# Optimization experiments

Measured on AMD Instinct MI355X. Metric: run time of the kernel, lower is better.

## Reference

```python
import jax, jax.numpy as jnp
from jax import lax
import numpy as np

C = 64      # channels
K = 3       # dynamic kernel size
N = 2       # batch
H = 256
W = 256
DOWN = 4    # avgpool factor


def _conv(x, w, b):
    # 'SAME' padding matches get_same_padding for odd kernels, dilation=1
    y = lax.conv_general_dilated(x, w, (1, 1), 'SAME',
                                 dimension_numbers=('NCHW', 'OIHW', 'NCHW'))
    return y + b[None, :, None, None]


def _resblock(x, w1, b1, w2, b2):
    out = jax.nn.leaky_relu(_conv(x, w1, b1), 0.1)
    return _conv(out, w2, b2) + x


def _block(x, ws1, bs1, ws2, bs2):
    # fixed small loop over 3 structurally distinct ResBlocks
    for i in range(ws1.shape[0]):
        x = _resblock(x, ws1[i], bs1[i], ws2[i], bs2[i])
    return x


def _avgpool(x, k):
    n, c, h, w = x.shape
    return x.reshape(n, c, h // k, k, w // k, k).mean(axis=(3, 5))


def _maxpool(x, k):
    n, c, h, w = x.shape
    return x.reshape(n, c, h // k, k, w // k, k).max(axis=(3, 5))


def _dyn_conv(x, wt, k):
    # per-pixel depthwise conv: out[n,c,h,w] = sum_{dh,dw} xpad[n,c,h+dh,w+dw] * wt[n, c*k*k + dh*k + dw, h, w]
    # (torch's unfold/permute flattening pairs feat tap (dh,dw) with kernel channel index dh*k+dw)
    n, c, h, w = x.shape
    pad = (k - 1) // 2
    xp = jnp.pad(x, ((0, 0), (0, 0), (pad, pad), (pad, pad)), mode='edge')  # replicate pad
    wr = wt.reshape(n, c, k * k, h, w)
    out = jnp.zeros_like(x)
    for dh in range(k):            # fixed 3x3 tap loop; avoids materializing the unfold tensor
        for dw in range(k):
            out = out + xp[:, :, dh:dh + h, dw:dw + w] * wr[:, :, dh * k + dw]
    return out


def setup_inputs() -> dict:
    key = jax.random.key(0)
    ks = jax.random.split(key, 11)
    s = 0.05  # small init so 6 residual blocks stay numerically tame
    return {
        'x': jax.random.normal(ks[0], (N, C, H, W), jnp.float32),
        'blk1_w1': jax.random.normal(ks[1], (3, C, C, K, K), jnp.float32) * s,
        'blk1_b1': jnp.zeros((3, C), jnp.float32),
        'blk1_w2': jax.random.normal(ks[2], (3, C, C, K, K), jnp.float32) * s,
        'blk1_b2': jnp.zeros((3, C), jnp.float32),
        'blk2_w1': jax.random.normal(ks[3], (3, C, C, K, K), jnp.float32) * s,
        'blk2_b1': jnp.zeros((3, C), jnp.float32),
        'blk2_w2': jax.random.normal(ks[4], (3, C, C, K, K), jnp.float32) * s,
        'blk2_b2': jnp.zeros((3, C), jnp.float32),
        'tok_w': jax.random.normal(ks[5], (K * K * C, C, 1, 1), jnp.float32) * s,
        'tok_b': jnp.zeros((K * K * C,), jnp.float32),
    }


def reference(x, blk1_w1, blk1_b1, blk1_w2, blk1_b2,
              blk2_w1, blk2_b1, blk2_w2, blk2_b2, tok_w, tok_b):
    y = _avgpool(x, DOWN)                                   # [N,C,H/4,W/4]
    y = _block(y, blk1_w1, blk1_b1, blk1_w2, blk1_b2)
    y = _maxpool(y, 2)                                      # [N,C,H/8,W/8]
    y = _block(y, blk2_w1, blk2_b1, blk2_w2, blk2_b2)
    wt = _conv(y, tok_w, tok_b)                             # [N,9C,H/8,W/8]
    n, ck2, hs, ws = wt.shape
    # F.interpolate(scale_factor=2*down, mode='bilinear', align_corners=False)
    wt = jax.image.resize(wt, (n, ck2, hs * 2 * DOWN, ws * 2 * DOWN), method='bilinear')
    return _dyn_conv(x, wt, K)
```

## Files before the change

kernel.cpp:

```cpp
#include <hip/hip_runtime.h>


__global__ __launch_bounds__(256) void avgpool4_k(const float* __restrict__ x,
                                                  float* __restrict__ y) {
    int idx = blockIdx.x * 256 + threadIdx.x;
    int wo = idx & 63;
    int ho = (idx >> 6) & 63;
    int cz = idx >> 12;
    const float* base = x + ((long)cz * 256 + ho * 4) * 256 + wo * 4;
    float s = 0.f;
#pragma unroll
    for (int r = 0; r < 4; ++r) {
        float4 v = *(const float4*)(base + r * 256);
        s += v.x + v.y + v.z + v.w;
    }
    y[idx] = s * 0.0625f;
}

__global__ __launch_bounds__(256) void maxpool2_k(const float* __restrict__ x,
                                                  float* __restrict__ y) {
    int idx = blockIdx.x * 256 + threadIdx.x;
    int wo = idx & 31;
    int ho = (idx >> 5) & 31;
    int cz = idx >> 10;
    const float* base = x + ((long)cz * 64 + ho * 2) * 64 + wo * 2;
    float a = base[0], b = base[1], c = base[64], d = base[65];
    y[idx] = fmaxf(fmaxf(a, b), fmaxf(c, d));
}

template <int S, int OCB>
__global__ __launch_bounds__(256) void conv3x3_t(
    const float* __restrict__ in, const float* __restrict__ wgt,
    const float* __restrict__ bias, const float* __restrict__ res,
    float* __restrict__ out, int lrelu) {
    __shared__ __align__(16) float s_w[64 * 9 * OCB];
    __shared__ float s_in[16 * 342];
    const int tid = threadIdx.x;
    const int tx = tid & 15;
    const int ty = tid >> 4;
    const int tw = blockIdx.x * 16, th = blockIdx.y * 16;
    const int n = blockIdx.z / (64 / OCB);
    const int oc0 = (blockIdx.z % (64 / OCB)) * OCB;

    for (int idx = tid; idx < OCB * 576; idx += 256) {
        int k = idx / 576;
        int r = idx - k * 576;
        int ci = r / 9;
        int tap = r - ci * 9;
        s_w[(ci * 9 + tap) * OCB + k] = wgt[(long)oc0 * 576 + idx];
    }

    constexpr int NLD = 21;
    int g_off[NLD];
    int l_off[NLD];
    unsigned vmask = 0;
#pragma unroll
    for (int j = 0; j < NLD; ++j) {
        int idx = tid + j * 256;
        int t = idx < 5184 ? idx : 5183;
        int ci = t / 324;
        int rem = t - ci * 324;
        int r = rem / 18;
        int c = rem - r * 18;
        int gh = th + r - 1, gw = tw + c - 1;
        if (idx < 5184 && (unsigned)gh < (unsigned)S && (unsigned)gw < (unsigned)S)
            vmask |= (1u << j);
        int ghc = gh < 0 ? 0 : (gh > S - 1 ? S - 1 : gh);
        int gwc = gw < 0 ? 0 : (gw > S - 1 ? S - 1 : gw);
        g_off[j] = ci * S * S + ghc * S + gwc;
        l_off[j] = ci * 342 + r * 19 + c;
    }

    const float* inb = in + (long)n * 64 * S * S;
    float pf[NLD];
#pragma unroll
    for (int j = 0; j < NLD; ++j) pf[j] = inb[g_off[j]];

    float acc[OCB];
#pragma unroll
    for (int k = 0; k < OCB; ++k) acc[k] = 0.f;

    for (int chunk = 0; chunk < 64; chunk += 16) {
        __syncthreads();
#pragma unroll
        for (int j = 0; j < NLD; ++j) {
            float v = ((vmask >> j) & 1u) ? pf[j] : 0.f;
            if (j < 20 || tid < 64) s_in[l_off[j]] = v;
        }
        __syncthreads();
        if (chunk + 16 < 64) {
            const float* nb = inb + (chunk + 16) * S * S;
#pragma unroll
            for (int j = 0; j < NLD; ++j) pf[j] = nb[g_off[j]];
        }
#pragma unroll 4
        for (int ci = 0; ci < 16; ++ci) {
            const float* sp = &s_in[ci * 342 + ty * 19 + tx];
            float xw[9];
#pragma unroll
            for (int r = 0; r < 3; ++r)
#pragma unroll
                for (int c = 0; c < 3; ++c)
                    xw[r * 3 + c] = sp[r * 19 + c];
            const float* wp = &s_w[(chunk + ci) * 9 * OCB];
#pragma unroll
            for (int t = 0; t < 9; ++t) {
                float xv = xw[t];
                if constexpr (OCB == 4) {
                    float4 wv = *(const float4*)&wp[t * 4];
                    acc[0] += xv * wv.x;
                    acc[1] += xv * wv.y;
                    acc[2] += xv * wv.z;
                    acc[3] += xv * wv.w;
                } else {
                    float2 wv = *(const float2*)&wp[t * 2];
                    acc[0] += xv * wv.x;
                    acc[1] += xv * wv.y;
                }
            }
        }
    }

    const int h = th + ty, w = tw + tx;
#pragma unroll
    for (int k = 0; k < OCB; ++k) {
        int oc = oc0 + k;
        float v = acc[k] + bias[oc];
        if (lrelu) v = v > 0.f ? v : 0.1f * v;
        long off = ((long)(n * 64 + oc) * S + h) * S + w;
        if (res) v += res[off];
        out[off] = v;
    }
}

__global__ __launch_bounds__(256) void conv1x1_k(
    const float* __restrict__ in, const float* __restrict__ w,
    const float* __restrict__ b, float* __restrict__ out) {
    __shared__ float s_in[32 * 256];
    __shared__ __align__(16) float s_w[64 * 8];
    const int tid = threadIdx.x;
    const int p0 = blockIdx.x * 256;
    const int cog = blockIdx.y;
    const int n = blockIdx.z;

    for (int idx = tid; idx < 512; idx += 256) {
        int j = idx >> 6;
        int ci = idx & 63;
        s_w[ci * 8 + j] = w[(long)cog * 512 + idx];
    }

    float acc[8];
#pragma unroll
    for (int i = 0; i < 8; ++i) acc[i] = b[cog * 8 + i];

    float pf[32];
#pragma unroll
    for (int i = 0; i < 32; ++i)
        pf[i] = in[(long)(n * 64 + i) * 1024 + p0 + tid];

    for (int chunk = 0; chunk < 64; chunk += 32) {
        __syncthreads();
#pragma unroll
        for (int i = 0; i < 32; ++i) s_in[i * 256 + tid] = pf[i];
        __syncthreads();
        if (chunk + 32 < 64) {
#pragma unroll
            for (int i = 0; i < 32; ++i)
                pf[i] = in[(long)(n * 64 + chunk + 32 + i) * 1024 + p0 + tid];
        }
#pragma unroll 4
        for (int ci = 0; ci < 32; ++ci) {
            float v = s_in[ci * 256 + tid];
            float4 w0 = *(const float4*)&s_w[(chunk + ci) * 8];
            float4 w1 = *(const float4*)&s_w[(chunk + ci) * 8 + 4];
            acc[0] += v * w0.x; acc[1] += v * w0.y;
            acc[2] += v * w0.z; acc[3] += v * w0.w;
            acc[4] += v * w1.x; acc[5] += v * w1.y;
            acc[6] += v * w1.z; acc[7] += v * w1.w;
        }
    }
#pragma unroll
    for (int oc = 0; oc < 8; ++oc)
        out[(long)(n * 576 + cog * 8 + oc) * 1024 + p0 + tid] = acc[oc];
}

__global__ __launch_bounds__(256) void dynconv_k(
    const float* __restrict__ x, const float* __restrict__ wt,
    float* __restrict__ out) {
    __shared__ __align__(16) float s_x[10 * 132];
    const int tid = threadIdx.x;
    const int tx = tid & 31;
    const int ty = tid >> 5;
    const int tw = (blockIdx.x & 1) * 128;
    const int th = (blockIdx.x >> 1) * 8;
    const int cz = blockIdx.y;

    const float* xb = x + (long)cz * 65536;
    for (int idx = tid; idx < 1300; idx += 256) {
        int r = idx / 130;
        int c = idx - r * 130;
        int gh = min(max(th + r - 1, 0), 255);
        int gw = min(max(tw + c - 1, 0), 255);
        s_x[r * 132 + c] = xb[gh * 256 + gw];
    }

    const int h = th + ty;
    const int wbase = tw + tx * 4;

    float src_h = h * 0.125f - 0.4375f;
    int h0 = (int)floorf(src_h);
    float fh = src_h - (float)h0;
    int h0c = min(max(h0, 0), 31), h1c = min(max(h0 + 1, 0), 31);
    float src_w = wbase * 0.125f - 0.4375f;
    int w0 = (int)floorf(src_w);
    float fw0 = src_w - (float)w0;
    int w0c = min(max(w0, 0), 31), w1c = min(max(w0 + 1, 0), 31);

    __syncthreads();

    float vals[3][6];
#pragma unroll
    for (int r = 0; r < 3; ++r) {
        const float* rp = &s_x[(ty + r) * 132 + tx * 4];
        float4 a = *(const float4*)rp;
        float2 b = *(const float2*)(rp + 4);
        vals[r][0] = a.x; vals[r][1] = a.y; vals[r][2] = a.z;
        vals[r][3] = a.w; vals[r][4] = b.x; vals[r][5] = b.y;
    }

    const float* wtb = wt + (long)cz * 9 * 1024;
    float acc[4] = {0.f, 0.f, 0.f, 0.f};
#pragma unroll
    for (int dh = 0; dh < 3; ++dh)
#pragma unroll
        for (int dw = 0; dw < 3; ++dw) {
            const float* p = wtb + (dh * 3 + dw) * 1024;
            float w00 = p[h0c * 32 + w0c], w01 = p[h0c * 32 + w1c];
            float w10 = p[h1c * 32 + w0c], w11 = p[h1c * 32 + w1c];
            float c0 = w00 + fh * (w10 - w00);
            float c1 = w01 + fh * (w11 - w01);
            float d = c1 - c0;
#pragma unroll
            for (int j = 0; j < 4; ++j) {
                float wv = c0 + (fw0 + 0.125f * j) * d;
                acc[j] += vals[dh][j + dw] * wv;
            }
        }

    float4 o;
    o.x = acc[0]; o.y = acc[1]; o.z = acc[2]; o.w = acc[3];
    *(float4*)&out[(long)cz * 65536 + h * 256 + wbase] = o;
}

extern "C" void kernel_launch(void* const* d_in, const int* in_sizes, int n_in,
                              void* d_out, int out_size, void* d_ws, size_t ws_size,
                              hipStream_t stream) {
    const float* x    = (const float*)d_in[0];
    const float* b1w1 = (const float*)d_in[1];
    const float* b1b1 = (const float*)d_in[2];
    const float* b1w2 = (const float*)d_in[3];
    const float* b1b2 = (const float*)d_in[4];
    const float* b2w1 = (const float*)d_in[5];
    const float* b2b1 = (const float*)d_in[6];
    const float* b2w2 = (const float*)d_in[7];
    const float* b2b2 = (const float*)d_in[8];
    const float* tokw = (const float*)d_in[9];
    const float* tokb = (const float*)d_in[10];
    float* out = (float*)d_out;
    float* ws = (float*)d_ws;

    float* A = ws;
    float* B = ws + 524288;
    float* T = ws + 1048576;
    float* P = ws;
    float* Q = ws + 131072;
    float* U = ws + 262144;
    float* WT = ws + 393216;

    const int WSZ = 64 * 64 * 9;

    avgpool4_k<<<2048, 256, 0, stream>>>(x, A);

    dim3 g64(4, 4, 32);
    conv3x3_t<64, 4><<<g64, 256, 0, stream>>>(A, b1w1 + 0 * WSZ, b1b1 + 0,   nullptr, T, 1);
    conv3x3_t<64, 4><<<g64, 256, 0, stream>>>(T, b1w2 + 0 * WSZ, b1b2 + 0,   A,       B, 0);
    conv3x3_t<64, 4><<<g64, 256, 0, stream>>>(B, b1w1 + 1 * WSZ, b1b1 + 64,  nullptr, T, 1);
    conv3x3_t<64, 4><<<g64, 256, 0, stream>>>(T, b1w2 + 1 * WSZ, b1b2 + 64,  B,       A, 0);
    conv3x3_t<64, 4><<<g64, 256, 0, stream>>>(A, b1w1 + 2 * WSZ, b1b1 + 128, nullptr, T, 1);
    conv3x3_t<64, 4><<<g64, 256, 0, stream>>>(T, b1w2 + 2 * WSZ, b1b2 + 128, A,       B, 0);

    maxpool2_k<<<512, 256, 0, stream>>>(B, P);

    dim3 g32(2, 2, 64);
    conv3x3_t<32, 2><<<g32, 256, 0, stream>>>(P, b2w1 + 0 * WSZ, b2b1 + 0,   nullptr, U, 1);
    conv3x3_t<32, 2><<<g32, 256, 0, stream>>>(U, b2w2 + 0 * WSZ, b2b2 + 0,   P,       Q, 0);
    conv3x3_t<32, 2><<<g32, 256, 0, stream>>>(Q, b2w1 + 1 * WSZ, b2b1 + 64,  nullptr, U, 1);
    conv3x3_t<32, 2><<<g32, 256, 0, stream>>>(U, b2w2 + 1 * WSZ, b2b2 + 64,  Q,       P, 0);
    conv3x3_t<32, 2><<<g32, 256, 0, stream>>>(P, b2w1 + 2 * WSZ, b2b1 + 128, nullptr, U, 1);
    conv3x3_t<32, 2><<<g32, 256, 0, stream>>>(U, b2w2 + 2 * WSZ, b2b2 + 128, P,       Q, 0);

    conv1x1_k<<<dim3(4, 72, 2), 256, 0, stream>>>(Q, tokw, tokb, WT);

    dynconv_k<<<dim3(64, 128), 256, 0, stream>>>(x, WT, out);
}
```

Measured before the change: 411.1 us.

## Split 64x64 convs over input-channel slices with fused partial-sum epilogue

Replaces the stage-1 3x3 convolutions with a split-K kernel. Each block handles 16 input channels for 4 output channels on a 32x32 tile and writes a partial sum. The next conv, or the maxpool, sums the four partials, then adds bias, leaky-relu and the residual while loading its input. The residual stream is written as a side output by the ocg==0 blocks. This raises block count and parallelism, and it removes the separate epilogue pass. The cost is extra global traffic, because four partial buffers are read by every consumer block, and the four-way summation is recomputed across output-channel groups.

After: 680.1 us. 1.65x slower.

```diff
diff --git a/kernel.cpp b/kernel.cpp
--- a/kernel.cpp
+++ b/kernel.cpp
@@ -17,15 +17,139 @@
     y[idx] = s * 0.0625f;
 }
 
-__global__ __launch_bounds__(256) void maxpool2_k(const float* __restrict__ x,
-                                                  float* __restrict__ y) {
+__global__ __launch_bounds__(256) void conv64s_k(
+    const float* __restrict__ in0, long pstride,
+    const float* __restrict__ sbias, int slrelu,
+    const float* __restrict__ sres,
+    float* __restrict__ sidew,
+    const float* __restrict__ wgt,
+    float* __restrict__ outp) {
+    __shared__ __align__(16) float s_x[8 * 34 * 36];
+    __shared__ __align__(16) float s_w[16 * 9 * 4];
+    const int tid = threadIdx.x;
+    const int b = blockIdx.x;
+    const int tg = b & 7;
+    const int slot = b >> 3;
+    const int n = tg >> 2;
+    const int tile = tg & 3;
+    const int tx0 = (tile & 1) * 32, ty0 = (tile >> 1) * 32;
+    const int ocg = slot & 15, ks = slot >> 4;
+    const int oc0 = ocg * 4;
+
+    for (int i = tid; i < 576; i += 256) {
+        int k = i / 144;
+        int rem = i - k * 144;
+        int ci = rem / 9;
+        int tap = rem - ci * 9;
+        s_w[(ci * 9 + tap) * 4 + k] =
+            wgt[(oc0 + k) * 576 + (ks * 16 + ci) * 9 + tap];
+    }
+
+    const int ntask = (tid < 16) ? 2 : 1;
+    int t_ci[2], t_j[2];
+    t_ci[0] = tid / 34;  t_j[0] = tid - t_ci[0] * 34;
+    t_ci[1] = (256 + tid) / 34; t_j[1] = (256 + tid) - t_ci[1] * 34;
+
+    const int tx = tid & 7;
+    const int ty = tid >> 3;
+    const int px0 = tx * 4;
+
+    float acc[4][4];
+#pragma unroll
+    for (int k = 0; k < 4; ++k)
+#pragma unroll
+        for (int p = 0; p < 4; ++p) acc[k][p] = 0.f;
+
+    for (int cc = 0; cc < 2; ++cc) {
+        if (cc) __syncthreads();
+        for (int t = 0; t < ntask; ++t) {
+            const int ci = t_ci[t], j = t_j[t];
+            const int ch = ks * 16 + cc * 8 + ci;
+            const int gcol = tx0 + j - 1;
+            const bool colin = (unsigned)gcol < 64u;
+            const long chbase = (long)(n * 64 + ch) * 4096;
+            float bch = 0.f;
+            if (pstride && colin) bch = sbias[ch];
+            float* sp = &s_x[(ci * 34) * 36 + j];
+#pragma unroll 2
+            for (int r = 0; r < 34; ++r) {
+                const int grow = ty0 + r - 1;
+                float v = 0.f;
+                if (colin && (unsigned)grow < 64u) {
+                    const long off = chbase + grow * 64 + gcol;
+                    if (pstride) {
+                        v = in0[off] + in0[off + pstride] +
+                            in0[off + 2 * pstride] + in0[off + 3 * pstride] + bch;
+                        if (slrelu) v = v > 0.f ? v : 0.1f * v;
+                        if (sres) v += sres[off];
+                        if (sidew && ocg == 0) sidew[off] = v;
+                    } else {
+                        v = in0[off];
+                    }
+                }
+                sp[r * 36] = v;
+            }
+        }
+        __syncthreads();
+#pragma unroll 2
+        for (int ci = 0; ci < 8; ++ci) {
+            float xr[3][6];
+#pragma unroll
+            for (int r3 = 0; r3 < 3; ++r3) {
+                const float* rp = &s_x[(ci * 34 + ty + r3) * 36 + px0];
+                float4 a = *(const float4*)rp;
+                float2 e = *(const float2*)(rp + 4);
+                xr[r3][0] = a.x; xr[r3][1] = a.y; xr[r3][2] = a.z;
+                xr[r3][3] = a.w; xr[r3][4] = e.x; xr[r3][5] = e.y;
+            }
+            const int cif = cc * 8 + ci;
+#pragma unroll
+            for (int dh = 0; dh < 3; ++dh)
+#pragma unroll
+                for (int dw = 0; dw < 3; ++dw) {
+                    float4 wv = *(const float4*)&s_w[(cif * 9 + dh * 3 + dw) * 4];
+#pragma unroll
+                    for (int p = 0; p < 4; ++p) {
+                        float xv = xr[dh][p + dw];
+                        acc[0][p] += xv * wv.x;
+                        acc[1][p] += xv * wv.y;
+                        acc[2][p] += xv * wv.z;
+                        acc[3][p] += xv * wv.w;
+                    }
+                }
+        }
+    }
+
+    const int gy = ty0 + ty, gx = tx0 + px0;
+#pragma unroll
+    for (int k = 0; k < 4; ++k) {
+        float4 v;
+        v.x = acc[k][0]; v.y = acc[k][1]; v.z = acc[k][2]; v.w = acc[k][3];
+        long off = (long)ks * 524288 +
+                   ((long)(n * 64 + oc0 + k) * 64 + gy) * 64 + gx;
+        *(float4*)&outp[off] = v;
+    }
+}
+
+__global__ __launch_bounds__(256) void maxpool_comb_k(
+    const float* __restrict__ Pb, const float* __restrict__ bias,
+    const float* __restrict__ res, float* __restrict__ P) {
     int idx = blockIdx.x * 256 + threadIdx.x;
     int wo = idx & 31;
     int ho = (idx >> 5) & 31;
     int cz = idx >> 10;
-    const float* base = x + ((long)cz * 64 + ho * 2) * 64 + wo * 2;
-    float a = base[0], b = base[1], c = base[64], d = base[65];
-    y[idx] = fmaxf(fmaxf(a, b), fmaxf(c, d));
+    float bch = bias[cz & 63];
+    float m = -3.4e38f;
+#pragma unroll
+    for (int dh = 0; dh < 2; ++dh)
+#pragma unroll
+        for (int dw = 0; dw < 2; ++dw) {
+            long off = ((long)cz * 64 + ho * 2 + dh) * 64 + wo * 2 + dw;
+            float y = Pb[off] + Pb[off + 524288] + Pb[off + 1048576] +
+                      Pb[off + 1572864] + bch + res[off];
+            m = fmaxf(m, y);
+        }
+    P[idx] = m;
 }
 
 template <int S, int OCB>
@@ -269,27 +393,29 @@
     float* out = (float*)d_out;
     float* ws = (float*)d_ws;
 
-    float* A = ws;
-    float* B = ws + 524288;
-    float* T = ws + 1048576;
-    float* P = ws;
-    float* Q = ws + 131072;
-    float* U = ws + 262144;
-    float* WT = ws + 393216;
+    float* A  = ws;
+    float* Y1 = ws + 524288;
+    float* Y2 = ws + 1048576;
+    float* Pa = ws + 1572864;
+    float* Pb = ws + 3670016;
+    float* P  = ws + 5767168;
+    float* Q  = ws + 5898240;
+    float* U  = ws + 6029312;
+    float* WT = ws + 6160384;
 
     const int WSZ = 64 * 64 * 9;
+    const long PS = 524288;
 
     avgpool4_k<<<2048, 256, 0, stream>>>(x, A);
 
-    dim3 g64(4, 4, 32);
-    conv3x3_t<64, 4><<<g64, 256, 0, stream>>>(A, b1w1 + 0 * WSZ, b1b1 + 0,   nullptr, T, 1);
-    conv3x3_t<64, 4><<<g64, 256, 0, stream>>>(T, b1w2 + 0 * WSZ, b1b2 + 0,   A,       B, 0);
-    conv3x3_t<64, 4><<<g64, 256, 0, stream>>>(B, b1w1 + 1 * WSZ, b1b1 + 64,  nullptr, T, 1);
-    conv3x3_t<64, 4><<<g64, 256, 0, stream>>>(T, b1w2 + 1 * WSZ, b1b2 + 64,  B,       A, 0);
-    conv3x3_t<64, 4><<<g64, 256, 0, stream>>>(A, b1w1 + 2 * WSZ, b1b1 + 128, nullptr, T, 1);
-    conv3x3_t<64, 4><<<g64, 256, 0, stream>>>(T, b1w2 + 2 * WSZ, b1b2 + 128, A,       B, 0);
-
-    maxpool2_k<<<512, 256, 0, stream>>>(B, P);
+    conv64s_k<<<512, 256, 0, stream>>>(A,  0,  nullptr,      0, nullptr, nullptr, b1w1 + 0 * WSZ, Pa);
+    conv64s_k<<<512, 256, 0, stream>>>(Pa, PS, b1b1 + 0,     1, nullptr, nullptr, b1w2 + 0 * WSZ, Pb);
+    conv64s_k<<<512, 256, 0, stream>>>(Pb, PS, b1b2 + 0,     0, A,       Y1,      b1w1 + 1 * WSZ, Pa);
+    conv64s_k<<<512, 256, 0, stream>>>(Pa, PS, b1b1 + 64,    1, nullptr, nullptr, b1w2 + 1 * WSZ, Pb);
+    conv64s_k<<<512, 256, 0, stream>>>(Pb, PS, b1b2 + 64,    0, Y1,      Y2,      b1w1 + 2 * WSZ, Pa);
+    conv64s_k<<<512, 256, 0, stream>>>(Pa, PS, b1b1 + 128,   1, nullptr, nullptr, b1w2 + 2 * WSZ, Pb);
+
+    maxpool_comb_k<<<512, 256, 0, stream>>>(Pb, b1b2 + 128, Y2, P);
 
     dim3 g32(2, 2, 64);
     conv3x3_t<32, 2><<<g32, 256, 0, stream>>>(P, b2w1 + 0 * WSZ, b2b1 + 0,   nullptr, U, 1);
```

## Split-K 3x3 convs with register-tiled outputs and separate combine kernels

Applied to the files above, without the earlier changes.

Replaces the per-layer 3x3 conv kernel with a split-K version: each block handles one slice of input channels, 16 output channels and a 16x16 tile, with every thread computing 4 output channels by 4 pixels in registers. The partial sums go to a workspace buffer and a separate combine kernel adds them along with bias, leaky ReLU and the residual. The last combine of block 1 is fused with the 2x2 maxpool. This is meant to raise the number of blocks and the arithmetic per shared-memory load for these small images. The cost is extra global traffic for the partials and twice as many kernel launches.

Result: faster. 387.9 us (-5.6%).

```diff
diff --git a/kernel.cpp b/kernel.cpp
--- a/kernel.cpp
+++ b/kernel.cpp
@@ -17,120 +17,149 @@
     y[idx] = s * 0.0625f;
 }
 
-__global__ __launch_bounds__(256) void maxpool2_k(const float* __restrict__ x,
-                                                  float* __restrict__ y) {
-    int idx = blockIdx.x * 256 + threadIdx.x;
-    int wo = idx & 31;
-    int ho = (idx >> 5) & 31;
-    int cz = idx >> 10;
-    const float* base = x + ((long)cz * 64 + ho * 2) * 64 + wo * 2;
-    float a = base[0], b = base[1], c = base[64], d = base[65];
-    y[idx] = fmaxf(fmaxf(a, b), fmaxf(c, d));
-}
-
-template <int S, int OCB>
-__global__ __launch_bounds__(256) void conv3x3_t(
+template <int S, int CIB>
+__global__ __launch_bounds__(256) void conv3x3s_k(
     const float* __restrict__ in, const float* __restrict__ wgt,
-    const float* __restrict__ bias, const float* __restrict__ res,
-    float* __restrict__ out, int lrelu) {
-    __shared__ __align__(16) float s_w[64 * 9 * OCB];
-    __shared__ float s_in[16 * 342];
+    float* __restrict__ outp) {
+    constexpr int KSN = 64 / CIB;
+    constexpr int TPS = S / 16;
+    constexpr int NT = TPS * TPS;
+    constexpr int TOT = CIB * 324;
+    constexpr int NLD = (TOT + 255) / 256;
+    constexpr int TAIL = TOT - (NLD - 1) * 256;
+    __shared__ float s_in[CIB * 360];
+    __shared__ __align__(16) float s_w[CIB * 144];
+
     const int tid = threadIdx.x;
-    const int tx = tid & 15;
-    const int ty = tid >> 4;
-    const int tw = blockIdx.x * 16, th = blockIdx.y * 16;
-    const int n = blockIdx.z / (64 / OCB);
-    const int oc0 = (blockIdx.z % (64 / OCB)) * OCB;
-
-    for (int idx = tid; idx < OCB * 576; idx += 256) {
-        int k = idx / 576;
-        int r = idx - k * 576;
-        int ci = r / 9;
-        int tap = r - ci * 9;
-        s_w[(ci * 9 + tap) * OCB + k] = wgt[(long)oc0 * 576 + idx];
-    }
-
-    constexpr int NLD = 21;
-    int g_off[NLD];
-    int l_off[NLD];
-    unsigned vmask = 0;
+    int z = blockIdx.x;
+    const int ks = z % KSN; z /= KSN;
+    const int ocg = z & 3; z >>= 2;
+    const int tile = z % NT;
+    const int n = z / NT;
+    const int th = (tile / TPS) * 16, tw = (tile % TPS) * 16;
+    const int oc0 = ocg * 16;
+
+    for (int i = tid; i < CIB * 144; i += 256) {
+        int k = i / (CIB * 9);
+        int rem = i - k * (CIB * 9);
+        s_w[rem * 16 + k] = wgt[(oc0 + k) * 576 + ks * (CIB * 9) + rem];
+    }
+
+    const float* inb = in + ((long)n * 64 + ks * CIB) * (S * S);
 #pragma unroll
     for (int j = 0; j < NLD; ++j) {
         int idx = tid + j * 256;
-        int t = idx < 5184 ? idx : 5183;
+        bool slot = (j < NLD - 1) || (tid < TAIL);
+        int t = slot ? idx : 0;
         int ci = t / 324;
         int rem = t - ci * 324;
         int r = rem / 18;
         int c = rem - r * 18;
         int gh = th + r - 1, gw = tw + c - 1;
-        if (idx < 5184 && (unsigned)gh < (unsigned)S && (unsigned)gw < (unsigned)S)
-            vmask |= (1u << j);
-        int ghc = gh < 0 ? 0 : (gh > S - 1 ? S - 1 : gh);
-        int gwc = gw < 0 ? 0 : (gw > S - 1 ? S - 1 : gw);
-        g_off[j] = ci * S * S + ghc * S + gwc;
-        l_off[j] = ci * 342 + r * 19 + c;
-    }
-
-    const float* inb = in + (long)n * 64 * S * S;
-    float pf[NLD];
-#pragma unroll
-    for (int j = 0; j < NLD; ++j) pf[j] = inb[g_off[j]];
-
-    float acc[OCB];
-#pragma unroll
-    for (int k = 0; k < OCB; ++k) acc[k] = 0.f;
-
-    for (int chunk = 0; chunk < 64; chunk += 16) {
-        __syncthreads();
-#pragma unroll
-        for (int j = 0; j < NLD; ++j) {
-            float v = ((vmask >> j) & 1u) ? pf[j] : 0.f;
-            if (j < 20 || tid < 64) s_in[l_off[j]] = v;
-        }
-        __syncthreads();
-        if (chunk + 16 < 64) {
-            const float* nb = inb + (chunk + 16) * S * S;
-#pragma unroll
-            for (int j = 0; j < NLD; ++j) pf[j] = nb[g_off[j]];
-        }
-#pragma unroll 4
-        for (int ci = 0; ci < 16; ++ci) {
-            const float* sp = &s_in[ci * 342 + ty * 19 + tx];
-            float xw[9];
-#pragma unroll
-            for (int r = 0; r < 3; ++r)
-#pragma unroll
-                for (int c = 0; c < 3; ++c)
-                    xw[r * 3 + c] = sp[r * 19 + c];
-            const float* wp = &s_w[(chunk + ci) * 9 * OCB];
-#pragma unroll
-            for (int t = 0; t < 9; ++t) {
-                float xv = xw[t];
-                if constexpr (OCB == 4) {
-                    float4 wv = *(const float4*)&wp[t * 4];
-                    acc[0] += xv * wv.x;
-                    acc[1] += xv * wv.y;
-                    acc[2] += xv * wv.z;
-                    acc[3] += xv * wv.w;
-                } else {
-                    float2 wv = *(const float2*)&wp[t * 2];
-                    acc[0] += xv * wv.x;
-                    acc[1] += xv * wv.y;
+        float v = 0.f;
+        if (slot && (unsigned)gh < (unsigned)S && (unsigned)gw < (unsigned)S)
+            v = inb[ci * (S * S) + gh * S + gw];
+        if (slot) s_in[ci * 360 + r * 20 + c] = v;
+    }
+    __syncthreads();
+
+    const int lane = tid & 63;
+    const int wid = tid >> 6;
+    const int tx4 = (lane & 3) * 4;
+    const int ty = lane >> 2;
+
+    float acc[4][4];
+#pragma unroll
+    for (int k = 0; k < 4; ++k)
+#pragma unroll
+        for (int p = 0; p < 4; ++p) acc[k][p] = 0.f;
+
+#pragma unroll 2
+    for (int ci = 0; ci < CIB; ++ci) {
+        float xr[3][6];
+#pragma unroll
+        for (int r = 0; r < 3; ++r) {
+            const float* rp = &s_in[ci * 360 + (ty + r) * 20 + tx4];
+            float4 a = *(const float4*)rp;
+            float2 b = *(const float2*)(rp + 4);
+            xr[r][0] = a.x; xr[r][1] = a.y; xr[r][2] = a.z;
+            xr[r][3] = a.w; xr[r][4] = b.x; xr[r][5] = b.y;
+        }
+#pragma unroll
+        for (int dh = 0; dh < 3; ++dh)
+#pragma unroll
+            for (int dw = 0; dw < 3; ++dw) {
+                float4 wv = *(const float4*)&s_w[(ci * 9 + dh * 3 + dw) * 16 + wid * 4];
+#pragma unroll
+                for (int p = 0; p < 4; ++p) {
+                    float xv = xr[dh][p + dw];
+                    acc[0][p] += xv * wv.x;
+                    acc[1][p] += xv * wv.y;
+                    acc[2][p] += xv * wv.z;
+                    acc[3][p] += xv * wv.w;
                 }
             }
-        }
-    }
-
-    const int h = th + ty, w = tw + tx;
-#pragma unroll
-    for (int k = 0; k < OCB; ++k) {
-        int oc = oc0 + k;
-        float v = acc[k] + bias[oc];
-        if (lrelu) v = v > 0.f ? v : 0.1f * v;
-        long off = ((long)(n * 64 + oc) * S + h) * S + w;
-        if (res) v += res[off];
-        out[off] = v;
-    }
+    }
+
+    const int gy = th + ty, gx = tw + tx4;
+    const long pstride = (long)2 * 64 * S * S;
+#pragma unroll
+    for (int k = 0; k < 4; ++k) {
+        float4 v;
+        v.x = acc[k][0]; v.y = acc[k][1]; v.z = acc[k][2]; v.w = acc[k][3];
+        long off = ks * pstride +
+                   ((long)(n * 64 + oc0 + wid * 4 + k)) * (S * S) + gy * S + gx;
+        *(float4*)&outp[off] = v;
+    }
+}
+
+template <int NP, int SSLOG, bool LRELU, bool RES>
+__global__ __launch_bounds__(256) void comb_k(
+    const float* __restrict__ P, const float* __restrict__ bias,
+    const float* __restrict__ res, float* __restrict__ out) {
+    const long pstride = (long)2 * 64 << SSLOG;
+    long base = ((long)blockIdx.x * 256 + threadIdx.x) * 4;
+    int c = (int)((base >> SSLOG) & 63);
+    float4 v = *(const float4*)&P[base];
+#pragma unroll
+    for (int p = 1; p < NP; ++p) {
+        float4 u = *(const float4*)&P[base + p * pstride];
+        v.x += u.x; v.y += u.y; v.z += u.z; v.w += u.w;
+    }
+    float b = bias[c];
+    v.x += b; v.y += b; v.z += b; v.w += b;
+    if (LRELU) {
+        v.x = v.x > 0.f ? v.x : 0.1f * v.x;
+        v.y = v.y > 0.f ? v.y : 0.1f * v.y;
+        v.z = v.z > 0.f ? v.z : 0.1f * v.z;
+        v.w = v.w > 0.f ? v.w : 0.1f * v.w;
+    }
+    if (RES) {
+        float4 r = *(const float4*)&res[base];
+        v.x += r.x; v.y += r.y; v.z += r.z; v.w += r.w;
+    }
+    *(float4*)&out[base] = v;
+}
+
+__global__ __launch_bounds__(256) void maxpool_comb_k(
+    const float* __restrict__ Pb, const float* __restrict__ bias,
+    const float* __restrict__ res, float* __restrict__ P) {
+    int idx = blockIdx.x * 256 + threadIdx.x;
+    int wo = idx & 31;
+    int ho = (idx >> 5) & 31;
+    int cz = idx >> 10;
+    float bch = bias[cz & 63];
+    float m = -3.4e38f;
+#pragma unroll
+    for (int dh = 0; dh < 2; ++dh)
+#pragma unroll
+        for (int dw = 0; dw < 2; ++dw) {
+            long off = ((long)cz * 64 + ho * 2 + dh) * 64 + wo * 2 + dw;
+            float y = Pb[off] + Pb[off + 524288] + Pb[off + 1048576] +
+                      Pb[off + 1572864] + bch + res[off];
+            m = fmaxf(m, y);
+        }
+    P[idx] = m;
 }
 
 __global__ __launch_bounds__(256) void conv1x1_k(
@@ -269,35 +298,48 @@
     float* out = (float*)d_out;
     float* ws = (float*)d_ws;
 
-    float* A = ws;
-    float* B = ws + 524288;
-    float* T = ws + 1048576;
-    float* P = ws;
-    float* Q = ws + 131072;
-    float* U = ws + 262144;
-    float* WT = ws + 393216;
+    float* X0 = ws;
+    float* X1 = ws + 524288;
+    float* T  = ws + 1048576;
+    float* P  = ws + 1572864;
+    float* Pm = ws + 3670016;
+    float* Q  = ws + 3801088;
+    float* U  = ws + 3932160;
+    float* WT = ws + 4063232;
 
     const int WSZ = 64 * 64 * 9;
 
-    avgpool4_k<<<2048, 256, 0, stream>>>(x, A);
-
-    dim3 g64(4, 4, 32);
-    conv3x3_t<64, 4><<<g64, 256, 0, stream>>>(A, b1w1 + 0 * WSZ, b1b1 + 0,   nullptr, T, 1);
-    conv3x3_t<64, 4><<<g64, 256, 0, stream>>>(T, b1w2 + 0 * WSZ, b1b2 + 0,   A,       B, 0);
-    conv3x3_t<64, 4><<<g64, 256, 0, stream>>>(B, b1w1 + 1 * WSZ, b1b1 + 64,  nullptr, T, 1);
-    conv3x3_t<64, 4><<<g64, 256, 0, stream>>>(T, b1w2 + 1 * WSZ, b1b2 + 64,  B,       A, 0);
-    conv3x3_t<64, 4><<<g64, 256, 0, stream>>>(A, b1w1 + 2 * WSZ, b1b1 + 128, nullptr, T, 1);
-    conv3x3_t<64, 4><<<g64, 256, 0, stream>>>(T, b1w2 + 2 * WSZ, b1b2 + 128, A,       B, 0);
-
-    maxpool2_k<<<512, 256, 0, stream>>>(B, P);
-
-    dim3 g32(2, 2, 64);
-    conv3x3_t<32, 2><<<g32, 256, 0, stream>>>(P, b2w1 + 0 * WSZ, b2b1 + 0,   nullptr, U, 1);
-    conv3x3_t<32, 2><<<g32, 256, 0, stream>>>(U, b2w2 + 0 * WSZ, b2b2 + 0,   P,       Q, 0);
-    conv3x3_t<32, 2><<<g32, 256, 0, stream>>>(Q, b2w1 + 1 * WSZ, b2b1 + 64,  nullptr, U, 1);
-    conv3x3_t<32, 2><<<g32, 256, 0, stream>>>(U, b2w2 + 1 * WSZ, b2b2 + 64,  Q,       P, 0);
-    conv3x3_t<32, 2><<<g32, 256, 0, stream>>>(P, b2w1 + 2 * WSZ, b2b1 + 128, nullptr, U, 1);
-    conv3x3_t<32, 2><<<g32, 256, 0, stream>>>(U, b2w2 + 2 * WSZ, b2b2 + 128, P,       Q, 0);
+    avgpool4_k<<<2048, 256, 0, stream>>>(x, X0);
+
+    conv3x3s_k<64, 16><<<512, 256, 0, stream>>>(X0, b1w1 + 0 * WSZ, P);
+    comb_k<4, 12, true,  false><<<512, 256, 0, stream>>>(P, b1b1 + 0, nullptr, T);
+    conv3x3s_k<64, 16><<<512, 256, 0, stream>>>(T, b1w2 + 0 * WSZ, P);
+    comb_k<4, 12, false, true ><<<512, 256, 0, stream>>>(P, b1b2 + 0, X0, X1);
+
+    conv3x3s_k<64, 16><<<512, 256, 0, stream>>>(X1, b1w1 + 1 * WSZ, P);
+    comb_k<4, 12, true,  false><<<512, 256, 0, stream>>>(P, b1b1 + 64, nullptr, T);
+    conv3x3s_k<64, 16><<<512, 256, 0, stream>>>(T, b1w2 + 1 * WSZ, P);
+    comb_k<4, 12, false, true ><<<512, 256, 0, stream>>>(P, b1b2 + 64, X1, X0);
+
+    conv3x3s_k<64, 16><<<512, 256, 0, stream>>>(X0, b1w1 + 2 * WSZ, P);
+    comb_k<4, 12, true,  false><<<512, 256, 0, stream>>>(P, b1b1 + 128, nullptr, T);
+    conv3x3s_k<64, 16><<<512, 256, 0, stream>>>(T, b1w2 + 2 * WSZ, P);
+    maxpool_comb_k<<<512, 256, 0, stream>>>(P, b1b2 + 128, X0, Pm);
+
+    conv3x3s_k<32, 8><<<256, 256, 0, stream>>>(Pm, b2w1 + 0 * WSZ, P);
+    comb_k<8, 10, true,  false><<<128, 256, 0, stream>>>(P, b2b1 + 0, nullptr, U);
+    conv3x3s_k<32, 8><<<256, 256, 0, stream>>>(U, b2w2 + 0 * WSZ, P);
+    comb_k<8, 10, false, true ><<<128, 256, 0, stream>>>(P, b2b2 + 0, Pm, Q);
+
+    conv3x3s_k<32, 8><<<256, 256, 0, stream>>>(Q, b2w1 + 1 * WSZ, P);
+    comb_k<8, 10, true,  false><<<128, 256, 0, stream>>>(P, b2b1 + 64, nullptr, U);
+    conv3x3s_k<32, 8><<<256, 256, 0, stream>>>(U, b2w2 + 1 * WSZ, P);
+    comb_k<8, 10, false, true ><<<128, 256, 0, stream>>>(P, b2b2 + 64, Q, Pm);
+
+    conv3x3s_k<32, 8><<<256, 256, 0, stream>>>(Pm, b2w1 + 2 * WSZ, P);
+    comb_k<8, 10, true,  false><<<128, 256, 0, stream>>>(P, b2b1 + 128, nullptr, U);
+    conv3x3s_k<32, 8><<<256, 256, 0, stream>>>(U, b2w2 + 2 * WSZ, P);
+    comb_k<8, 10, false, true ><<<128, 256, 0, stream>>>(P, b2b2 + 128, Pm, Q);
 
     conv1x1_k<<<dim3(4, 72, 2), 256, 0, stream>>>(Q, tokw, tokb, WT);
 
```
